# Optimization experiments

Measured on AMD Instinct MI355X. Metric: run time of the kernel, lower is better.

The kernel has to match this reference:

```python
import jax, jax.numpy as jnp
import numpy as np

N_TYPES = 6
NUM_HEADS = 8
MAX_SEQ = 50
LN_EPS = 1e-5
NEG_SLOPE = 0.2


def layer_norm(x, g, b):
    m = x.mean(-1, keepdims=True)
    v = ((x - m) ** 2).mean(-1, keepdims=True)
    return (x - m) / jnp.sqrt(v + LN_EPS) * g + b


def setup_inputs() -> dict:
    key = jax.random.key(0)
    N, E, D = 20000, 200000, 128  # nodes, edges, input_dim==hidden_dim
    ks = jax.random.split(key, 64)
    it = iter(ks)

    def w(shape):
        return jax.random.normal(next(it), shape, jnp.float32) / np.sqrt(shape[-2] if len(shape) > 1 else shape[-1]).astype(np.float32)

    inp = {}
    inp['x'] = jax.random.normal(next(it), (N, D), jnp.float32)
    inp['edge_index'] = jax.random.randint(next(it), (2, E), 0, N)
    inp['node_types'] = jax.random.randint(next(it), (N,), 0, N_TYPES)
    inp['temporal_positions'] = jax.random.randint(next(it), (N,), 0, MAX_SEQ)
    # CrossDomainGAT params
    inp['gat_Wq'] = w((D, D)); inp['gat_Wk'] = w((D, D)); inp['gat_Wv'] = w((D, D))
    inp['gat_Wo'] = w((D, D)); inp['gat_bo'] = jnp.zeros((D,), jnp.float32)
    inp['gat_g'] = jnp.ones((D,), jnp.float32); inp['gat_b'] = jnp.zeros((D,), jnp.float32)
    # SchemaAwareGCN params
    inp['gcn_Wt'] = w((N_TYPES, D, D)); inp['gcn_bt'] = jnp.zeros((N_TYPES, D), jnp.float32)
    inp['gcn_mW1'] = w((2 * D, D)); inp['gcn_mb1'] = jnp.zeros((D,), jnp.float32)
    inp['gcn_mW2'] = w((D, D)); inp['gcn_mb2'] = jnp.zeros((D,), jnp.float32)
    inp['gcn_aW1'] = w((D, D)); inp['gcn_ab1'] = jnp.zeros((D,), jnp.float32)
    inp['gcn_aW2'] = w((D, D)); inp['gcn_ab2'] = jnp.zeros((D,), jnp.float32)
    inp['gcn_Wo'] = w((D, D)); inp['gcn_bo'] = jnp.zeros((D,), jnp.float32)
    inp['gcn_g'] = jnp.ones((D,), jnp.float32); inp['gcn_b'] = jnp.zeros((D,), jnp.float32)
    # TemporalReasoningGNN params (no turn_boundaries -> LSTM/attention path skipped)
    inp['tmp_emb'] = jax.random.normal(next(it), (MAX_SEQ, D), jnp.float32)
    inp['tmp_W1'] = w((2 * D, D)); inp['tmp_b1'] = jnp.zeros((D,), jnp.float32)
    inp['tmp_W2'] = w((D, D)); inp['tmp_b2'] = jnp.zeros((D,), jnp.float32)
    inp['tmp_Wo'] = w((D, D)); inp['tmp_bo'] = jnp.zeros((D,), jnp.float32)
    inp['tmp_g'] = jnp.ones((D,), jnp.float32); inp['tmp_b'] = jnp.zeros((D,), jnp.float32)
    # Unified fusion (concat of 3 branches -> hidden) + LayerNorm
    inp['fus_W'] = w((3 * D, D)); inp['fus_b'] = jnp.zeros((D,), jnp.float32)
    inp['fus_g'] = jnp.ones((D,), jnp.float32); inp['fus_be'] = jnp.zeros((D,), jnp.float32)
    return inp


def _gat(x, row, col, Wq, Wk, Wv, Wo, bo, g, b):
    N, D = x.shape
    Dh = D // NUM_HEADS
    Q = (x @ Wq).reshape(N, NUM_HEADS, Dh)
    K = (x @ Wk).reshape(N, NUM_HEADS, Dh)
    V = (x @ Wv).reshape(N, NUM_HEADS, Dh)
    # edge-wise multi-head attention scores [E, H]
    scores = (Q[row] * K[col]).sum(-1) / np.sqrt(Dh).astype(np.float32)
    scores = jax.nn.leaky_relu(scores, NEG_SLOPE)
    # segment softmax over incoming edges of each col node
    mx = jax.ops.segment_max(scores, col, num_segments=N)
    ex = jnp.exp(scores - mx[col])
    sm = jax.ops.segment_sum(ex, col, num_segments=N)
    probs = ex / sm[col]
    wv = probs[:, :, None] * V[row]  # [E, H, Dh]
    out = jax.ops.segment_sum(wv.reshape(len(row), D), col, num_segments=N)
    out = out @ Wo + bo
    return layer_norm(out + x, g, b)


def _mlp2(z, W1, b1, W2, b2):
    return jax.nn.relu(z @ W1 + b1) @ W2 + b2


def _gcn(x, row, col, node_types, Wt, bt, mW1, mb1, mW2, mb2, aW1, ab1, aW2, ab2, Wo, bo, g, b):
    N, D = x.shape
    h = jnp.zeros((N, D), x.dtype)
    for t in range(N_TYPES):  # fixed small type count
        h = h + jnp.where((node_types == t)[:, None], x @ Wt[t] + bt[t], 0.0)
    messages = _mlp2(jnp.concatenate([h[row], h[col]], axis=1), mW1, mb1, mW2, mb2)
    agg = jax.ops.segment_sum(messages, col, num_segments=N)
    h = h + _mlp2(agg, aW1, ab1, aW2, ab2)
    h = h @ Wo + bo
    return layer_norm(h + x, g, b)


def _temporal(x, row, col, tpos, emb, W1, b1, W2, b2, Wo, bo, g, b):
    N, D = x.shape
    h = x + emb[jnp.clip(tpos, 0, MAX_SEQ - 1)]
    messages = _mlp2(jnp.concatenate([h[row], h[col]], axis=1), W1, b1, W2, b2)
    h = h + jax.ops.segment_sum(messages, col, num_segments=N)
    h = h @ Wo + bo
    return layer_norm(h, g, b)


def reference(x, edge_index, node_types, temporal_positions,
              gat_Wq, gat_Wk, gat_Wv, gat_Wo, gat_bo, gat_g, gat_b,
              gcn_Wt, gcn_bt, gcn_mW1, gcn_mb1, gcn_mW2, gcn_mb2,
              gcn_aW1, gcn_ab1, gcn_aW2, gcn_ab2, gcn_Wo, gcn_bo, gcn_g, gcn_b,
              tmp_emb, tmp_W1, tmp_b1, tmp_W2, tmp_b2, tmp_Wo, tmp_bo, tmp_g, tmp_b,
              fus_W, fus_b, fus_g, fus_be):
    row, col = edge_index[0], edge_index[1]
    o_gat = _gat(x, row, col, gat_Wq, gat_Wk, gat_Wv, gat_Wo, gat_bo, gat_g, gat_b)
    o_gcn = _gcn(x, row, col, node_types, gcn_Wt, gcn_bt, gcn_mW1, gcn_mb1, gcn_mW2, gcn_mb2,
                 gcn_aW1, gcn_ab1, gcn_aW2, gcn_ab2, gcn_Wo, gcn_bo, gcn_g, gcn_b)
    o_tmp = _temporal(x, row, col, temporal_positions, tmp_emb, tmp_W1, tmp_b1, tmp_W2, tmp_b2,
                      tmp_Wo, tmp_bo, tmp_g, tmp_b)
    fused = jnp.concatenate([o_gat, o_gcn, o_tmp], axis=-1) @ fus_W + fus_b
    return layer_norm(fused, fus_g, fus_be)
```

## Files before the change

kernel.cpp:

```cpp
#include <hip/hip_runtime.h>

using u32 = unsigned int;
using s64 = long long;

__global__ __launch_bounds__(64) void k_detect13(const u32* __restrict__ ei,
                                                 const u32* __restrict__ nt,
                                                 const u32* __restrict__ tp,
                                                 u32* __restrict__ flags) {
    if (blockIdx.x != 0 || threadIdx.x != 0) return;
    bool e64 = true, n64 = true, t64 = true;
    for (int k = 0; k < 64; ++k) {
        if (ei[2 * k + 1] != 0u) e64 = false;
        if (nt[2 * k + 1] != 0u) n64 = false;
        if (tp[2 * k + 1] != 0u) t64 = false;
    }
    flags[0] = e64 ? 1u : 0u;
    flags[1] = n64 ? 1u : 0u;
    flags[2] = t64 ? 1u : 0u;
}

__global__ __launch_bounds__(256) void k_cvt13(const void* __restrict__ src,
                                               int* __restrict__ dst, long long n,
                                               const u32* __restrict__ flags, int fidx) {
    long long i = (long long)blockIdx.x * 256 + threadIdx.x;
    if (i >= n) return;
    dst[i] = flags[fidx] ? (int)((const s64*)src)[i] : ((const int*)src)[i];
}

__global__ __launch_bounds__(256) void kz13(float* __restrict__ p, long long n) {
    long long i = (long long)blockIdx.x * 256 + threadIdx.x;
    if (i < n) p[i] = 0.f;
}
__global__ __launch_bounds__(256) void kz_i(int* __restrict__ p, int n) {
    int i = blockIdx.x * 256 + threadIdx.x;
    if (i < n) p[i] = 0;
}

__global__ __launch_bounds__(256) void k_hist(const int* __restrict__ ei, int E,
                                              int* __restrict__ cnt) {
    int e = blockIdx.x * 256 + threadIdx.x;
    if (e < E) atomicAdd(&cnt[ei[E + e]], 1);
}

__global__ __launch_bounds__(1024) void k_scan(const int* __restrict__ cnt,
                                               int* __restrict__ offA, int N) {
    __shared__ int part[1024];
    int t = threadIdx.x;
    int C = (N + 1023) >> 10;
    int beg = t * C, end = beg + C; if (end > N) end = N;
    int s = 0;
    for (int k = beg; k < end; ++k) s += cnt[k];
    part[t] = s; __syncthreads();
    for (int o = 1; o < 1024; o <<= 1) {
        int v = (t >= o) ? part[t - o] : 0;
        __syncthreads();
        part[t] += v;
        __syncthreads();
    }
    int base = (t == 0) ? 0 : part[t - 1];
    for (int k = beg; k < end; ++k) { offA[k] = base; base += cnt[k]; }
    if (t == 1023) offA[N] = part[1023];
}

__global__ __launch_bounds__(256) void k_scatter(const int* __restrict__ ei, int E,
                                                 const int* __restrict__ offA,
                                                 int* __restrict__ cur,
                                                 int* __restrict__ srow,
                                                 int* __restrict__ sedge) {
    int e = blockIdx.x * 256 + threadIdx.x;
    if (e >= E) return;
    int col = ei[E + e];
    int p = offA[col] + atomicAdd(&cur[col], 1);
    srow[p] = ei[e];
    sedge[p] = e;
}

__global__ __launch_bounds__(256) void k_thist(const int* __restrict__ nt, int N,
                                               int* __restrict__ tcnt) {
    __shared__ int lc[6];
    if (threadIdx.x < 6) lc[threadIdx.x] = 0;
    __syncthreads();
    int i = blockIdx.x * 256 + threadIdx.x;
    if (i < N) {
        int t = nt[i]; t = (t < 0 || t > 5) ? 0 : t;
        atomicAdd(&lc[t], 1);
    }
    __syncthreads();
    if (threadIdx.x < 6 && lc[threadIdx.x] > 0) atomicAdd(&tcnt[threadIdx.x], lc[threadIdx.x]);
}

__global__ __launch_bounds__(64) void k_tscan(const int* __restrict__ tcnt,
                                              int* __restrict__ toff) {
    if (threadIdx.x != 0 || blockIdx.x != 0) return;
    int s = 0;
    for (int t = 0; t < 6; ++t) { toff[t] = s; s += tcnt[t]; }
    toff[6] = s;
}

__global__ __launch_bounds__(256) void k_tscatter(const int* __restrict__ nt, int N,
                                                  const int* __restrict__ toff,
                                                  int* __restrict__ tcur,
                                                  int* __restrict__ perm) {
    __shared__ int lc[6], gb[6];
    if (threadIdx.x < 6) lc[threadIdx.x] = 0;
    __syncthreads();
    int i = blockIdx.x * 256 + threadIdx.x;
    int t = 0, lr = 0;
    if (i < N) {
        t = nt[i]; t = (t < 0 || t > 5) ? 0 : t;
        lr = atomicAdd(&lc[t], 1);
    }
    __syncthreads();
    if (threadIdx.x < 6 && lc[threadIdx.x] > 0)
        gb[threadIdx.x] = atomicAdd(&tcur[threadIdx.x], lc[threadIdx.x]);
    __syncthreads();
    if (i < N) perm[toff[t] + gb[t] + lr] = i;
}

__device__ __forceinline__ float2 ld2(const float* p) { return *(const float2*)p; }
__device__ __forceinline__ void st2(float* p, float2 v) { *(float2*)p = v; }
__device__ __forceinline__ float4 ld4(const float* p) { return *(const float4*)p; }
__device__ __forceinline__ void st4(float* p, float4 v) { *(float4*)p = v; }
__device__ __forceinline__ void fma4(float4& a, float s, float4 w) {
    a.x = fmaf(s, w.x, a.x); a.y = fmaf(s, w.y, a.y);
    a.z = fmaf(s, w.z, a.z); a.w = fmaf(s, w.w, a.w);
}

__device__ __forceinline__ float redrow(float s) {
#pragma unroll
    for (int o = 1; o < 32; o <<= 1) s += __shfl_xor(s, o);
    return s;
}


__device__ __forceinline__ void mmT(float4 (&acc)[4], const float* xs,
                                    const float* __restrict__ W, int tn, int tc) {
#pragma unroll 2
    for (int k4 = 0; k4 < 32; ++k4) {
        float4 w0 = ld4(W + (size_t)(k4 * 4 + 0) * 128 + tc * 4);
        float4 w1 = ld4(W + (size_t)(k4 * 4 + 1) * 128 + tc * 4);
        float4 w2 = ld4(W + (size_t)(k4 * 4 + 2) * 128 + tc * 4);
        float4 w3 = ld4(W + (size_t)(k4 * 4 + 3) * 128 + tc * 4);
#pragma unroll
        for (int j = 0; j < 4; ++j) {
            float4 xv = ld4(xs + (tn * 4 + j) * 128 + k4 * 4);
            fma4(acc[j], xv.x, w0); fma4(acc[j], xv.y, w1);
            fma4(acc[j], xv.z, w2); fma4(acc[j], xv.w, w3);
        }
    }
}

__device__ __forceinline__ float4 lnrow(float4 v, const float* g, const float* b, int tc) {
    float m = redrow(v.x + v.y + v.z + v.w) * 0.0078125f;
    float4 d = make_float4(v.x - m, v.y - m, v.z - m, v.w - m);
    float var = redrow(d.x * d.x + d.y * d.y + d.z * d.z + d.w * d.w) * 0.0078125f;
    float r = rsqrtf(var + 1e-5f);
    float4 gg = ld4(g + tc * 4), bb = ld4(b + tc * 4);
    return make_float4(d.x * r * gg.x + bb.x, d.y * r * gg.y + bb.y,
                       d.z * r * gg.z + bb.z, d.w * r * gg.w + bb.w);
}

__device__ __forceinline__ void stage32(float* xs, const float* src, int i0, int N) {
    int t = threadIdx.x;
#pragma unroll
    for (int ii = 0; ii < 4; ++ii) {
        int idx = t + ii * 256;
        int r = idx >> 5, c = idx & 31;
        int node = i0 + r; if (node >= N) node = N - 1;
        st4(xs + r * 128 + c * 4, ld4(src + (size_t)node * 128 + c * 4));
    }
}

__device__ __forceinline__ void xstore(float* xs, const float4 (&v)[4], int tn, int tc) {
#pragma unroll
    for (int j = 0; j < 4; ++j) st4(xs + (tn * 4 + j) * 128 + tc * 4, v[j]);
}

__global__ __launch_bounds__(256) void k_qkvT(const float* __restrict__ x,
                                              const float* __restrict__ Wq,
                                              const float* __restrict__ Wk,
                                              const float* __restrict__ Wv,
                                              float* __restrict__ big, int N) {
    __shared__ float xs[32 * 128];
    int t = threadIdx.x, tn = t >> 5, tc = t & 31;
    int i0 = blockIdx.x * 32;
    stage32(xs, x, i0, N);
    __syncthreads();
    float4 acc[4];
    const float* Ws[3] = {Wq, Wk, Wv};
#pragma unroll
    for (int m = 0; m < 3; ++m) {
#pragma unroll
        for (int j = 0; j < 4; ++j) acc[j] = make_float4(0.f, 0.f, 0.f, 0.f);
        mmT(acc, xs, Ws[m], tn, tc);
#pragma unroll
        for (int j = 0; j < 4; ++j) {
            int node = i0 + tn * 4 + j;
            if (node < N) st4(big + (size_t)node * 384 + m * 128 + tc * 4, acc[j]);
        }
    }
}

__global__ __launch_bounds__(256) void k_gat_smB(const float* __restrict__ big,
                                                 const int* __restrict__ ei, int E,
                                                 float* __restrict__ scores,
                                                 float* __restrict__ sm) {
    long long t = (long long)blockIdx.x * 256 + threadIdx.x;
    if (t >= (long long)E * 8) return;
    int e = (int)(t >> 3), h = (int)(t & 7);
    int row = ei[e], col = ei[E + e];
    const float4* q = (const float4*)(big + (size_t)row * 384 + h * 16);
    const float4* kk = (const float4*)(big + (size_t)col * 384 + 128 + h * 16);
    float s = 0.f;
#pragma unroll
    for (int d = 0; d < 4; ++d) {
        float4 a = q[d], b = kk[d];
        s += a.x * b.x + a.y * b.y + a.z * b.z + a.w * b.w;
    }
    s *= 0.25f;
    s = s > 0.f ? s : 0.2f * s;
    float ex = expf(s);
    scores[t] = ex;
    atomicAdd(&sm[(size_t)col * 8 + h], ex);
}

__global__ __launch_bounds__(256) void k_wvS2(const float* __restrict__ big,
                                              const float* __restrict__ scores,
                                              const float* __restrict__ sm,
                                              const int* __restrict__ srow,
                                              const int* __restrict__ sedge,
                                              const int* __restrict__ offA,
                                              float* __restrict__ agg, int N) {
    int l = threadIdx.x & 63;
    int col = blockIdx.x * 4 + (threadIdx.x >> 6);
    if (col >= N) return;
    int h = l >> 3;
    float sv = sm[(size_t)col * 8 + h];
    float ism = sv != 0.f ? 1.f / sv : 0.f;
    float ax = 0.f, ay = 0.f;
    int p = offA[col], pe = offA[col + 1];
    for (; p + 2 <= pe; p += 2) {
        int e0 = sedge[p], r0 = srow[p], e1 = sedge[p + 1], r1 = srow[p + 1];
        float pr0 = scores[(size_t)e0 * 8 + h] * ism;
        float pr1 = scores[(size_t)e1 * 8 + h] * ism;
        float2 v0 = ld2(big + (size_t)r0 * 384 + 256 + 2 * l);
        float2 v1 = ld2(big + (size_t)r1 * 384 + 256 + 2 * l);
        ax = fmaf(pr0, v0.x, ax); ay = fmaf(pr0, v0.y, ay);
        ax = fmaf(pr1, v1.x, ax); ay = fmaf(pr1, v1.y, ay);
    }
    for (; p < pe; ++p) {
        int e = sedge[p], r = srow[p];
        float pr = scores[(size_t)e * 8 + h] * ism;
        float2 v = ld2(big + (size_t)r * 384 + 256 + 2 * l);
        ax = fmaf(pr, v.x, ax); ay = fmaf(pr, v.y, ay);
    }
    st2(agg + (size_t)col * 128 + 2 * l, make_float2(ax, ay));
}

__global__ __launch_bounds__(256) void k_ep_gatT(const float* __restrict__ x,
                                                 const float* __restrict__ agg,
                                                 const float* __restrict__ Wo,
                                                 const float* __restrict__ bo,
                                                 const float* __restrict__ g,
                                                 const float* __restrict__ b,
                                                 const float* __restrict__ fusW,
                                                 const float* __restrict__ fus_b,
                                                 float* __restrict__ fused, int N) {
    __shared__ float xs[32 * 128];
    int t = threadIdx.x, tn = t >> 5, tc = t & 31;
    int i0 = blockIdx.x * 32;
    stage32(xs, agg, i0, N);
    __syncthreads();
    float4 acc[4];
    float4 bo4 = ld4(bo + tc * 4);
#pragma unroll
    for (int j = 0; j < 4; ++j) acc[j] = bo4;
    mmT(acc, xs, Wo, tn, tc);
    float4 o[4];
#pragma unroll
    for (int j = 0; j < 4; ++j) {
        int node = i0 + tn * 4 + j; if (node >= N) node = N - 1;
        float4 xr = ld4(x + (size_t)node * 128 + tc * 4);
        float4 v = make_float4(acc[j].x + xr.x, acc[j].y + xr.y,
                               acc[j].z + xr.z, acc[j].w + xr.w);
        o[j] = lnrow(v, g, b, tc);
    }
    __syncthreads();
    xstore(xs, o, tn, tc);
    __syncthreads();
    float4 fb4 = ld4(fus_b + tc * 4);
#pragma unroll
    for (int j = 0; j < 4; ++j) acc[j] = fb4;
    mmT(acc, xs, fusW, tn, tc);
#pragma unroll
    for (int j = 0; j < 4; ++j) {
        int node = i0 + tn * 4 + j;
        if (node < N) st4(fused + (size_t)node * 128 + tc * 4, acc[j]);
    }
}

__global__ __launch_bounds__(256) void k_hgcnT(const float* __restrict__ x,
                                               const int* __restrict__ nt,
                                               const int* __restrict__ perm,
                                               const float* __restrict__ Wt,
                                               const float* __restrict__ bt,
                                               float* __restrict__ h_gcn, int N) {
    __shared__ float xs[32 * 128];
    int t = threadIdx.x, tn = t >> 5, tc = t & 31;
    int i0 = blockIdx.x * 32;
#pragma unroll
    for (int ii = 0; ii < 4; ++ii) {
        int idx = t + ii * 256;
        int r = idx >> 5, c = idx & 31;
        int q = i0 + r; if (q >= N) q = N - 1;
        int node = perm[q];
        st4(xs + r * 128 + c * 4, ld4(x + (size_t)node * 128 + c * 4));
    }
    __syncthreads();
    int qa = i0; if (qa >= N) qa = N - 1;
    int qb = i0 + 31; if (qb >= N) qb = N - 1;
    int t0 = nt[perm[qa]]; t0 = (t0 < 0 || t0 > 5) ? 0 : t0;
    int t1 = nt[perm[qb]]; t1 = (t1 < 0 || t1 > 5) ? 0 : t1;
    float4 acc[4];
    if (t0 == t1) {
#pragma unroll
        for (int j = 0; j < 4; ++j) acc[j] = ld4(bt + t0 * 128 + tc * 4);
        mmT(acc, xs, Wt + (size_t)t0 * 16384, tn, tc);
    } else {
#pragma unroll
        for (int j = 0; j < 4; ++j) {
            int q = i0 + tn * 4 + j; if (q >= N) q = N - 1;
            int tt = nt[perm[q]]; tt = (tt < 0 || tt > 5) ? 0 : tt;
            const float* W = Wt + (size_t)tt * 16384;
            float4 a = ld4(bt + tt * 128 + tc * 4);
#pragma unroll 2
            for (int k4 = 0; k4 < 32; ++k4) {
                float4 xv = ld4(xs + (tn * 4 + j) * 128 + k4 * 4);
                float4 w0 = ld4(W + (size_t)(k4 * 4 + 0) * 128 + tc * 4);
                float4 w1 = ld4(W + (size_t)(k4 * 4 + 1) * 128 + tc * 4);
                float4 w2 = ld4(W + (size_t)(k4 * 4 + 2) * 128 + tc * 4);
                float4 w3 = ld4(W + (size_t)(k4 * 4 + 3) * 128 + tc * 4);
                fma4(a, xv.x, w0); fma4(a, xv.y, w1);
                fma4(a, xv.z, w2); fma4(a, xv.w, w3);
            }
            acc[j] = a;
        }
    }
#pragma unroll
    for (int j = 0; j < 4; ++j) {
        int q = i0 + tn * 4 + j;
        if (q < N) st4(h_gcn + (size_t)perm[q] * 128 + tc * 4, acc[j]);
    }
}

__global__ __launch_bounds__(256) void k_preT(const float* __restrict__ h,
                                              const float* __restrict__ emb,
                                              const int* __restrict__ tpos,
                                              const float* __restrict__ W1,
                                              const float* __restrict__ b1,
                                              float* __restrict__ Pa,
                                              float* __restrict__ Pb, int N, int mode) {
    __shared__ float xs[32 * 128];
    int t = threadIdx.x, tn = t >> 5, tc = t & 31;
    int i0 = blockIdx.x * 32;
#pragma unroll
    for (int ii = 0; ii < 4; ++ii) {
        int idx = t + ii * 256;
        int r = idx >> 5, c = idx & 31;
        int node = i0 + r; if (node >= N) node = N - 1;
        float4 v = ld4(h + (size_t)node * 128 + c * 4);
        if (mode) {
            int tp = tpos[node]; tp = tp < 0 ? 0 : (tp > 49 ? 49 : tp);
            float4 e = ld4(emb + tp * 128 + c * 4);
            v.x += e.x; v.y += e.y; v.z += e.z; v.w += e.w;
        }
        st4(xs + r * 128 + c * 4, v);
    }
    __syncthreads();
    float4 acc[4];
#pragma unroll
    for (int j = 0; j < 4; ++j) acc[j] = make_float4(0.f, 0.f, 0.f, 0.f);
    mmT(acc, xs, W1, tn, tc);
#pragma unroll
    for (int j = 0; j < 4; ++j) {
        int node = i0 + tn * 4 + j;
        if (node < N) st4(Pa + (size_t)node * 128 + tc * 4, acc[j]);
    }
    float4 b14 = ld4(b1 + tc * 4);
#pragma unroll
    for (int j = 0; j < 4; ++j) acc[j] = b14;
    mmT(acc, xs, W1 + (size_t)128 * 128, tn, tc);
#pragma unroll
    for (int j = 0; j < 4; ++j) {
        int node = i0 + tn * 4 + j;
        if (node < N) st4(Pb + (size_t)node * 128 + tc * 4, acc[j]);
    }
}

__global__ __launch_bounds__(256) void k_rsum2(const float* __restrict__ Pa,
                                               const float* __restrict__ Pb,
                                               const int* __restrict__ srow,
                                               const int* __restrict__ offA,
                                               float* __restrict__ s, int N) {
    int l = threadIdx.x & 63;
    int col = blockIdx.x * 4 + (threadIdx.x >> 6);
    if (col >= N) return;
    float2 pb = ld2(Pb + (size_t)col * 128 + 2 * l);
    float ax = 0.f, ay = 0.f;
    int p = offA[col], pe = offA[col + 1];
    for (; p + 4 <= pe; p += 4) {
        int r0 = srow[p], r1 = srow[p + 1], r2 = srow[p + 2], r3 = srow[p + 3];
        float2 a0 = ld2(Pa + (size_t)r0 * 128 + 2 * l);
        float2 a1 = ld2(Pa + (size_t)r1 * 128 + 2 * l);
        float2 a2 = ld2(Pa + (size_t)r2 * 128 + 2 * l);
        float2 a3 = ld2(Pa + (size_t)r3 * 128 + 2 * l);
        ax += fmaxf(a0.x + pb.x, 0.f) + fmaxf(a1.x + pb.x, 0.f)
            + fmaxf(a2.x + pb.x, 0.f) + fmaxf(a3.x + pb.x, 0.f);
        ay += fmaxf(a0.y + pb.y, 0.f) + fmaxf(a1.y + pb.y, 0.f)
            + fmaxf(a2.y + pb.y, 0.f) + fmaxf(a3.y + pb.y, 0.f);
    }
    for (; p < pe; ++p) {
        int r = srow[p];
        float2 a = ld2(Pa + (size_t)r * 128 + 2 * l);
        ax += fmaxf(a.x + pb.x, 0.f);
        ay += fmaxf(a.y + pb.y, 0.f);
    }
    st2(s + (size_t)col * 128 + 2 * l, make_float2(ax, ay));
}

__global__ __launch_bounds__(256) void k_ep_gcnT(const float* __restrict__ x,
                                                 const float* __restrict__ h_gcn,
                                                 const float* __restrict__ s,
                                                 const int* __restrict__ offA,
                                                 const float* __restrict__ W2,
                                                 const float* __restrict__ b2,
                                                 const float* __restrict__ aW1,
                                                 const float* __restrict__ ab1,
                                                 const float* __restrict__ aW2,
                                                 const float* __restrict__ ab2,
                                                 const float* __restrict__ Wo,
                                                 const float* __restrict__ bo,
                                                 const float* __restrict__ g,
                                                 const float* __restrict__ b,
                                                 const float* __restrict__ fusW,
                                                 float* __restrict__ fused, int N) {
    __shared__ float xs[32 * 128];
    int t = threadIdx.x, tn = t >> 5, tc = t & 31;
    int i0 = blockIdx.x * 32;
    int node[4];
#pragma unroll
    for (int j = 0; j < 4; ++j) {
        node[j] = i0 + tn * 4 + j; if (node[j] >= N) node[j] = N - 1;
    }
    stage32(xs, s, i0, N);
    __syncthreads();
    float4 acc[4];
    float4 b24 = ld4(b2 + tc * 4);
#pragma unroll
    for (int j = 0; j < 4; ++j) {
        float deg = (float)(offA[node[j] + 1] - offA[node[j]]);
        acc[j] = make_float4(deg * b24.x, deg * b24.y, deg * b24.z, deg * b24.w);
    }
    mmT(acc, xs, W2, tn, tc);
    __syncthreads();
    xstore(xs, acc, tn, tc);
    __syncthreads();
    float4 a14 = ld4(ab1 + tc * 4);
#pragma unroll
    for (int j = 0; j < 4; ++j) acc[j] = a14;
    mmT(acc, xs, aW1, tn, tc);
#pragma unroll
    for (int j = 0; j < 4; ++j) {
        acc[j].x = fmaxf(acc[j].x, 0.f); acc[j].y = fmaxf(acc[j].y, 0.f);
        acc[j].z = fmaxf(acc[j].z, 0.f); acc[j].w = fmaxf(acc[j].w, 0.f);
    }
    __syncthreads();
    xstore(xs, acc, tn, tc);
    __syncthreads();
    float4 a24 = ld4(ab2 + tc * 4);
#pragma unroll
    for (int j = 0; j < 4; ++j) acc[j] = a24;
    mmT(acc, xs, aW2, tn, tc);
#pragma unroll
    for (int j = 0; j < 4; ++j) {
        float4 hg = ld4(h_gcn + (size_t)node[j] * 128 + tc * 4);
        acc[j].x += hg.x; acc[j].y += hg.y; acc[j].z += hg.z; acc[j].w += hg.w;
    }
    __syncthreads();
    xstore(xs, acc, tn, tc);
    __syncthreads();
    float4 bo4 = ld4(bo + tc * 4);
#pragma unroll
    for (int j = 0; j < 4; ++j) acc[j] = bo4;
    mmT(acc, xs, Wo, tn, tc);
    float4 o[4];
#pragma unroll
    for (int j = 0; j < 4; ++j) {
        float4 xr = ld4(x + (size_t)node[j] * 128 + tc * 4);
        float4 v = make_float4(acc[j].x + xr.x, acc[j].y + xr.y,
                               acc[j].z + xr.z, acc[j].w + xr.w);
        o[j] = lnrow(v, g, b, tc);
    }
    __syncthreads();
    xstore(xs, o, tn, tc);
    __syncthreads();
#pragma unroll
    for (int j = 0; j < 4; ++j) acc[j] = ld4(fused + (size_t)node[j] * 128 + tc * 4);
    mmT(acc, xs, fusW + (size_t)128 * 128, tn, tc);
#pragma unroll
    for (int j = 0; j < 4; ++j) {
        int q = i0 + tn * 4 + j;
        if (q < N) st4(fused + (size_t)q * 128 + tc * 4, acc[j]);
    }
}

__global__ __launch_bounds__(256) void k_ep_tmpT(const float* __restrict__ x,
                                                 const float* __restrict__ emb,
                                                 const int* __restrict__ tpos,
                                                 const float* __restrict__ s,
                                                 const int* __restrict__ offA,
                                                 const float* __restrict__ W2,
                                                 const float* __restrict__ b2,
                                                 const float* __restrict__ Wo,
                                                 const float* __restrict__ bo,
                                                 const float* __restrict__ g,
                                                 const float* __restrict__ b,
                                                 const float* __restrict__ fusW,
                                                 const float* __restrict__ fused,
                                                 const float* __restrict__ fg,
                                                 const float* __restrict__ fbe,
                                                 float* __restrict__ out, int N) {
    __shared__ float xs[32 * 128];
    int t = threadIdx.x, tn = t >> 5, tc = t & 31;
    int i0 = blockIdx.x * 32;
    int node[4];
#pragma unroll
    for (int j = 0; j < 4; ++j) {
        node[j] = i0 + tn * 4 + j; if (node[j] >= N) node[j] = N - 1;
    }
    stage32(xs, s, i0, N);
    __syncthreads();
    float4 acc[4];
    float4 b24 = ld4(b2 + tc * 4);
#pragma unroll
    for (int j = 0; j < 4; ++j) {
        float deg = (float)(offA[node[j] + 1] - offA[node[j]]);
        acc[j] = make_float4(deg * b24.x, deg * b24.y, deg * b24.z, deg * b24.w);
    }
    mmT(acc, xs, W2, tn, tc);
#pragma unroll
    for (int j = 0; j < 4; ++j) {
        int tp = tpos[node[j]]; tp = tp < 0 ? 0 : (tp > 49 ? 49 : tp);
        float4 xr = ld4(x + (size_t)node[j] * 128 + tc * 4);
        float4 e = ld4(emb + tp * 128 + tc * 4);
        acc[j].x += xr.x + e.x; acc[j].y += xr.y + e.y;
        acc[j].z += xr.z + e.z; acc[j].w += xr.w + e.w;
    }
    __syncthreads();
    xstore(xs, acc, tn, tc);
    __syncthreads();
    float4 bo4 = ld4(bo + tc * 4);
#pragma unroll
    for (int j = 0; j < 4; ++j) acc[j] = bo4;
    mmT(acc, xs, Wo, tn, tc);
    float4 o[4];
#pragma unroll
    for (int j = 0; j < 4; ++j) o[j] = lnrow(acc[j], g, b, tc);
    __syncthreads();
    xstore(xs, o, tn, tc);
    __syncthreads();
#pragma unroll
    for (int j = 0; j < 4; ++j) acc[j] = ld4(fused + (size_t)node[j] * 128 + tc * 4);
    mmT(acc, xs, fusW + (size_t)256 * 128, tn, tc);
#pragma unroll
    for (int j = 0; j < 4; ++j) {
        float4 res = lnrow(acc[j], fg, fbe, tc);
        int q = i0 + tn * 4 + j;
        if (q < N) st4(out + (size_t)q * 128 + tc * 4, res);
    }
}

extern "C" void kernel_launch(void* const* d_in, const int* in_sizes, int n_in, void* d_out,
                              int out_size, void* d_ws, size_t ws_size, hipStream_t stream) {
    (void)n_in; (void)out_size; (void)ws_size;
    const float* x = (const float*)d_in[0];
    const float* gat_Wq = (const float*)d_in[4];
    const float* gat_Wk = (const float*)d_in[5];
    const float* gat_Wv = (const float*)d_in[6];
    const float* gat_Wo = (const float*)d_in[7];
    const float* gat_bo = (const float*)d_in[8];
    const float* gat_g = (const float*)d_in[9];
    const float* gat_b = (const float*)d_in[10];
    const float* gcn_Wt = (const float*)d_in[11];
    const float* gcn_bt = (const float*)d_in[12];
    const float* gcn_mW1 = (const float*)d_in[13];
    const float* gcn_mb1 = (const float*)d_in[14];
    const float* gcn_mW2 = (const float*)d_in[15];
    const float* gcn_mb2 = (const float*)d_in[16];
    const float* gcn_aW1 = (const float*)d_in[17];
    const float* gcn_ab1 = (const float*)d_in[18];
    const float* gcn_aW2 = (const float*)d_in[19];
    const float* gcn_ab2 = (const float*)d_in[20];
    const float* gcn_Wo = (const float*)d_in[21];
    const float* gcn_bo = (const float*)d_in[22];
    const float* gcn_g = (const float*)d_in[23];
    const float* gcn_b = (const float*)d_in[24];
    const float* tmp_emb = (const float*)d_in[25];
    const float* tmp_W1 = (const float*)d_in[26];
    const float* tmp_b1 = (const float*)d_in[27];
    const float* tmp_W2 = (const float*)d_in[28];
    const float* tmp_b2 = (const float*)d_in[29];
    const float* tmp_Wo = (const float*)d_in[30];
    const float* tmp_bo = (const float*)d_in[31];
    const float* tmp_g = (const float*)d_in[32];
    const float* tmp_b = (const float*)d_in[33];
    const float* fus_W = (const float*)d_in[34];
    const float* fus_b = (const float*)d_in[35];
    const float* fus_g = (const float*)d_in[36];
    const float* fus_be = (const float*)d_in[37];

    int N = in_sizes[0] / 128;
    int E = in_sizes[1] / 2;

    float* ws = (float*)d_ws;
    float* big = ws;
    float* fused = ws;
    float* h_gcn = ws + (size_t)128 * N;
    float* Pa = ws + (size_t)256 * N;
    float* Pb = ws + (size_t)384 * N;
    float* agg = ws + (size_t)512 * N;
    float* sm = ws + (size_t)640 * N;
    u32* flags = (u32*)(ws + (size_t)648 * N);
    int* ei32 = (int*)(flags + 16);
    int* nt32 = ei32 + (size_t)2 * E;
    int* tp32 = nt32 + N;
    float* scores = (float*)(tp32 + N);
    int* offA = (int*)(scores + (size_t)8 * E);
    int* cur = offA + (N + 1);
    int* srow = cur + N;
    int* sedge = srow + E;
    int* tcnt = sedge + E;
    int* toff = tcnt + 6;
    int* tcur = toff + 7;
    int* perm = cur;

    k_detect13<<<1, 64, 0, stream>>>((const u32*)d_in[1], (const u32*)d_in[2],
                                     (const u32*)d_in[3], flags);
    long long nEI = (long long)2 * E;
    k_cvt13<<<(int)((nEI + 255) / 256), 256, 0, stream>>>(d_in[1], ei32, nEI, flags, 0);
    k_cvt13<<<(N + 255) / 256, 256, 0, stream>>>(d_in[2], nt32, N, flags, 1);
    k_cvt13<<<(N + 255) / 256, 256, 0, stream>>>(d_in[3], tp32, N, flags, 2);

    int gE = (E + 255) / 256;
    int gN = (N + 255) / 256;
    int gT = (N + 31) / 32;
    int gC = (N + 3) / 4;
    int gE8 = (int)(((long long)E * 8 + 255) / 256);

    kz_i<<<gN, 256, 0, stream>>>(cur, N);
    k_hist<<<gE, 256, 0, stream>>>(ei32, E, cur);
    k_scan<<<1, 1024, 0, stream>>>(cur, offA, N);
    kz_i<<<gN, 256, 0, stream>>>(cur, N);
    k_scatter<<<gE, 256, 0, stream>>>(ei32, E, offA, cur, srow, sedge);

    kz_i<<<1, 32, 0, stream>>>(tcnt, 19);
    k_thist<<<gN, 256, 0, stream>>>(nt32, N, tcnt);
    k_tscan<<<1, 64, 0, stream>>>(tcnt, toff);
    k_tscatter<<<gN, 256, 0, stream>>>(nt32, N, toff, tcur, perm);

    kz13<<<(int)(((long long)8 * N + 255) / 256), 256, 0, stream>>>(sm, (long long)8 * N);
    k_qkvT<<<gT, 256, 0, stream>>>(x, gat_Wq, gat_Wk, gat_Wv, big, N);
    k_gat_smB<<<gE8, 256, 0, stream>>>(big, ei32, E, scores, sm);
    k_wvS2<<<gC, 256, 0, stream>>>(big, scores, sm, srow, sedge, offA, agg, N);
    k_ep_gatT<<<gT, 256, 0, stream>>>(x, agg, gat_Wo, gat_bo, gat_g, gat_b,
                                      fus_W, fus_b, fused, N);

    k_hgcnT<<<gT, 256, 0, stream>>>(x, nt32, perm, gcn_Wt, gcn_bt, h_gcn, N);
    k_preT<<<gT, 256, 0, stream>>>(h_gcn, nullptr, nullptr, gcn_mW1, gcn_mb1, Pa, Pb, N, 0);
    k_rsum2<<<gC, 256, 0, stream>>>(Pa, Pb, srow, offA, agg, N);
    k_ep_gcnT<<<gT, 256, 0, stream>>>(x, h_gcn, agg, offA, gcn_mW2, gcn_mb2,
                                      gcn_aW1, gcn_ab1, gcn_aW2, gcn_ab2,
                                      gcn_Wo, gcn_bo, gcn_g, gcn_b, fus_W, fused, N);

    k_preT<<<gT, 256, 0, stream>>>(x, tmp_emb, tp32, tmp_W1, tmp_b1, Pa, Pb, N, 1);
    k_rsum2<<<gC, 256, 0, stream>>>(Pa, Pb, srow, offA, agg, N);
    k_ep_tmpT<<<gT, 256, 0, stream>>>(x, tmp_emb, tp32, agg, offA, tmp_W2, tmp_b2,
                                      tmp_Wo, tmp_bo, tmp_g, tmp_b, fus_W, fused,
                                      fus_g, fus_be, (float*)d_out, N);
}
```

Measured before the change: 546.2 us.

## Stage weight matrices in LDS with register prefetch of the next weight

Replaces the per-thread global-memory weight reads in the dense 32x128x128 tiles with a full 64KB LDS copy of each weight matrix. Each stage stores the prefetched registers into LDS, then starts the global loads for the next weight before computing, so those loads overlap with the math. The intent is to cut repeated global and L2 weight traffic and hide load latency. In exchange each block needs about 80KB of LDS and 64 extra registers per thread, which reduces occupancy.

```diff
diff --git a/kernel.cpp b/kernel.cpp
--- a/kernel.cpp
+++ b/kernel.cpp
@@ -133,7 +133,41 @@
 }
 
 
-__device__ __forceinline__ void mmT(float4 (&acc)[4], const float* xs,
+__device__ __forceinline__ void wpre(float4 (&wreg)[16], const float* __restrict__ Wg) {
+    int t = threadIdx.x;
+#pragma unroll
+    for (int i = 0; i < 16; ++i) wreg[i] = ld4(Wg + (size_t)(t + i * 256) * 4);
+}
+
+__device__ __forceinline__ void mmP(float4 (&acc)[4], float* xs, float* wl,
+                                    float4 (&wreg)[16], const float* __restrict__ Wnext,
+                                    const float4* xin, int tn, int tc) {
+    int t = threadIdx.x;
+    __syncthreads();
+#pragma unroll
+    for (int i = 0; i < 16; ++i) st4(wl + (size_t)(t + i * 256) * 4, wreg[i]);
+    if (xin) {
+#pragma unroll
+        for (int j = 0; j < 4; ++j) st4(xs + (tn * 4 + j) * 128 + tc * 4, xin[j]);
+    }
+    if (Wnext) wpre(wreg, Wnext);
+    __syncthreads();
+#pragma unroll 2
+    for (int k4 = 0; k4 < 32; ++k4) {
+        float4 w0 = ld4(wl + (k4 * 4 + 0) * 128 + tc * 4);
+        float4 w1 = ld4(wl + (k4 * 4 + 1) * 128 + tc * 4);
+        float4 w2 = ld4(wl + (k4 * 4 + 2) * 128 + tc * 4);
+        float4 w3 = ld4(wl + (k4 * 4 + 3) * 128 + tc * 4);
+#pragma unroll
+        for (int j = 0; j < 4; ++j) {
+            float4 xv = ld4(xs + (tn * 4 + j) * 128 + k4 * 4);
+            fma4(acc[j], xv.x, w0); fma4(acc[j], xv.y, w1);
+            fma4(acc[j], xv.z, w2); fma4(acc[j], xv.w, w3);
+        }
+    }
+}
+
+__device__ __forceinline__ void mmG(float4 (&acc)[4], const float* xs,
                                     const float* __restrict__ W, int tn, int tc) {
 #pragma unroll 2
     for (int k4 = 0; k4 < 32; ++k4) {
@@ -171,28 +205,25 @@
     }
 }
 
-__device__ __forceinline__ void xstore(float* xs, const float4 (&v)[4], int tn, int tc) {
-#pragma unroll
-    for (int j = 0; j < 4; ++j) st4(xs + (tn * 4 + j) * 128 + tc * 4, v[j]);
-}
-
 __global__ __launch_bounds__(256) void k_qkvT(const float* __restrict__ x,
                                               const float* __restrict__ Wq,
                                               const float* __restrict__ Wk,
                                               const float* __restrict__ Wv,
                                               float* __restrict__ big, int N) {
     __shared__ float xs[32 * 128];
+    __shared__ float wl[128 * 128];
     int t = threadIdx.x, tn = t >> 5, tc = t & 31;
     int i0 = blockIdx.x * 32;
     stage32(xs, x, i0, N);
-    __syncthreads();
+    float4 wreg[16];
+    wpre(wreg, Wq);
+    const float* Ws[3] = {Wq, Wk, Wv};
     float4 acc[4];
-    const float* Ws[3] = {Wq, Wk, Wv};
 #pragma unroll
     for (int m = 0; m < 3; ++m) {
 #pragma unroll
         for (int j = 0; j < 4; ++j) acc[j] = make_float4(0.f, 0.f, 0.f, 0.f);
-        mmT(acc, xs, Ws[m], tn, tc);
+        mmP(acc, xs, wl, wreg, m < 2 ? Ws[m + 1] : nullptr, nullptr, tn, tc);
 #pragma unroll
         for (int j = 0; j < 4; ++j) {
             int node = i0 + tn * 4 + j;
@@ -267,15 +298,17 @@
                                                  const float* __restrict__ fus_b,
                                                  float* __restrict__ fused, int N) {
     __shared__ float xs[32 * 128];
+    __shared__ float wl[128 * 128];
     int t = threadIdx.x, tn = t >> 5, tc = t & 31;
     int i0 = blockIdx.x * 32;
     stage32(xs, agg, i0, N);
-    __syncthreads();
+    float4 wreg[16];
+    wpre(wreg, Wo);
     float4 acc[4];
     float4 bo4 = ld4(bo + tc * 4);
 #pragma unroll
     for (int j = 0; j < 4; ++j) acc[j] = bo4;
-    mmT(acc, xs, Wo, tn, tc);
+    mmP(acc, xs, wl, wreg, fusW, nullptr, tn, tc);
     float4 o[4];
 #pragma unroll
     for (int j = 0; j < 4; ++j) {
@@ -285,13 +318,10 @@
                                acc[j].z + xr.z, acc[j].w + xr.w);
         o[j] = lnrow(v, g, b, tc);
     }
-    __syncthreads();
-    xstore(xs, o, tn, tc);
-    __syncthreads();
     float4 fb4 = ld4(fus_b + tc * 4);
 #pragma unroll
     for (int j = 0; j < 4; ++j) acc[j] = fb4;
-    mmT(acc, xs, fusW, tn, tc);
+    mmP(acc, xs, wl, wreg, nullptr, o, tn, tc);
 #pragma unroll
     for (int j = 0; j < 4; ++j) {
         int node = i0 + tn * 4 + j;
@@ -306,6 +336,7 @@
                                                const float* __restrict__ bt,
                                                float* __restrict__ h_gcn, int N) {
     __shared__ float xs[32 * 128];
+    __shared__ float wl[128 * 128];
     int t = threadIdx.x, tn = t >> 5, tc = t & 31;
     int i0 = blockIdx.x * 32;
 #pragma unroll
@@ -316,17 +347,19 @@
         int node = perm[q];
         st4(xs + r * 128 + c * 4, ld4(x + (size_t)node * 128 + c * 4));
     }
-    __syncthreads();
     int qa = i0; if (qa >= N) qa = N - 1;
     int qb = i0 + 31; if (qb >= N) qb = N - 1;
     int t0 = nt[perm[qa]]; t0 = (t0 < 0 || t0 > 5) ? 0 : t0;
     int t1 = nt[perm[qb]]; t1 = (t1 < 0 || t1 > 5) ? 0 : t1;
     float4 acc[4];
     if (t0 == t1) {
+        float4 wreg[16];
+        wpre(wreg, Wt + (size_t)t0 * 16384);
 #pragma unroll
         for (int j = 0; j < 4; ++j) acc[j] = ld4(bt + t0 * 128 + tc * 4);
-        mmT(acc, xs, Wt + (size_t)t0 * 16384, tn, tc);
+        mmP(acc, xs, wl, wreg, nullptr, nullptr, tn, tc);
     } else {
+        __syncthreads();
 #pragma unroll
         for (int j = 0; j < 4; ++j) {
             int q = i0 + tn * 4 + j; if (q >= N) q = N - 1;
@@ -361,6 +394,7 @@
                                               float* __restrict__ Pa,
                                               float* __restrict__ Pb, int N, int mode) {
     __shared__ float xs[32 * 128];
+    __shared__ float wl[128 * 128];
     int t = threadIdx.x, tn = t >> 5, tc = t & 31;
     int i0 = blockIdx.x * 32;
 #pragma unroll
@@ -376,11 +410,12 @@
         }
         st4(xs + r * 128 + c * 4, v);
     }
-    __syncthreads();
+    float4 wreg[16];
+    wpre(wreg, W1);
     float4 acc[4];
 #pragma unroll
     for (int j = 0; j < 4; ++j) acc[j] = make_float4(0.f, 0.f, 0.f, 0.f);
-    mmT(acc, xs, W1, tn, tc);
+    mmP(acc, xs, wl, wreg, W1 + (size_t)128 * 128, nullptr, tn, tc);
 #pragma unroll
     for (int j = 0; j < 4; ++j) {
         int node = i0 + tn * 4 + j;
@@ -389,7 +424,7 @@
     float4 b14 = ld4(b1 + tc * 4);
 #pragma unroll
     for (int j = 0; j < 4; ++j) acc[j] = b14;
-    mmT(acc, xs, W1 + (size_t)128 * 128, tn, tc);
+    mmP(acc, xs, wl, wreg, nullptr, nullptr, tn, tc);
 #pragma unroll
     for (int j = 0; j < 4; ++j) {
         int node = i0 + tn * 4 + j;
@@ -445,6 +480,7 @@
                                                  const float* __restrict__ fusW,
                                                  float* __restrict__ fused, int N) {
     __shared__ float xs[32 * 128];
+    __shared__ float wl[128 * 128];
     int t = threadIdx.x, tn = t >> 5, tc = t & 31;
     int i0 = blockIdx.x * 32;
     int node[4];
@@ -453,64 +489,57 @@
         node[j] = i0 + tn * 4 + j; if (node[j] >= N) node[j] = N - 1;
     }
     stage32(xs, s, i0, N);
-    __syncthreads();
-    float4 acc[4];
+    float4 wreg[16];
+    wpre(wreg, W2);
+    float4 t1[4];
     float4 b24 = ld4(b2 + tc * 4);
 #pragma unroll
     for (int j = 0; j < 4; ++j) {
         float deg = (float)(offA[node[j] + 1] - offA[node[j]]);
-        acc[j] = make_float4(deg * b24.x, deg * b24.y, deg * b24.z, deg * b24.w);
-    }
-    mmT(acc, xs, W2, tn, tc);
-    __syncthreads();
-    xstore(xs, acc, tn, tc);
-    __syncthreads();
+        t1[j] = make_float4(deg * b24.x, deg * b24.y, deg * b24.z, deg * b24.w);
+    }
+    mmP(t1, xs, wl, wreg, aW1, nullptr, tn, tc);
+    float4 u[4];
     float4 a14 = ld4(ab1 + tc * 4);
 #pragma unroll
-    for (int j = 0; j < 4; ++j) acc[j] = a14;
-    mmT(acc, xs, aW1, tn, tc);
-#pragma unroll
-    for (int j = 0; j < 4; ++j) {
-        acc[j].x = fmaxf(acc[j].x, 0.f); acc[j].y = fmaxf(acc[j].y, 0.f);
-        acc[j].z = fmaxf(acc[j].z, 0.f); acc[j].w = fmaxf(acc[j].w, 0.f);
-    }
-    __syncthreads();
-    xstore(xs, acc, tn, tc);
-    __syncthreads();
+    for (int j = 0; j < 4; ++j) u[j] = a14;
+    mmP(u, xs, wl, wreg, aW2, t1, tn, tc);
+#pragma unroll
+    for (int j = 0; j < 4; ++j) {
+        u[j].x = fmaxf(u[j].x, 0.f); u[j].y = fmaxf(u[j].y, 0.f);
+        u[j].z = fmaxf(u[j].z, 0.f); u[j].w = fmaxf(u[j].w, 0.f);
+    }
+    float4 z3[4];
     float4 a24 = ld4(ab2 + tc * 4);
 #pragma unroll
-    for (int j = 0; j < 4; ++j) acc[j] = a24;
-    mmT(acc, xs, aW2, tn, tc);
+    for (int j = 0; j < 4; ++j) z3[j] = a24;
+    mmP(z3, xs, wl, wreg, Wo, u, tn, tc);
 #pragma unroll
     for (int j = 0; j < 4; ++j) {
         float4 hg = ld4(h_gcn + (size_t)node[j] * 128 + tc * 4);
-        acc[j].x += hg.x; acc[j].y += hg.y; acc[j].z += hg.z; acc[j].w += hg.w;
-    }
-    __syncthreads();
-    xstore(xs, acc, tn, tc);
-    __syncthreads();
+        z3[j].x += hg.x; z3[j].y += hg.y; z3[j].z += hg.z; z3[j].w += hg.w;
+    }
+    float4 d[4];
     float4 bo4 = ld4(bo + tc * 4);
 #pragma unroll
-    for (int j = 0; j < 4; ++j) acc[j] = bo4;
-    mmT(acc, xs, Wo, tn, tc);
+    for (int j = 0; j < 4; ++j) d[j] = bo4;
+    mmP(d, xs, wl, wreg, fusW + (size_t)128 * 128, z3, tn, tc);
     float4 o[4];
 #pragma unroll
     for (int j = 0; j < 4; ++j) {
         float4 xr = ld4(x + (size_t)node[j] * 128 + tc * 4);
-        float4 v = make_float4(acc[j].x + xr.x, acc[j].y + xr.y,
-                               acc[j].z + xr.z, acc[j].w + xr.w);
+        float4 v = make_float4(d[j].x + xr.x, d[j].y + xr.y,
+                               d[j].z + xr.z, d[j].w + xr.w);
         o[j] = lnrow(v, g, b, tc);
     }
-    __syncthreads();
-    xstore(xs, o, tn, tc);
-    __syncthreads();
-#pragma unroll
-    for (int j = 0; j < 4; ++j) acc[j] = ld4(fused + (size_t)node[j] * 128 + tc * 4);
-    mmT(acc, xs, fusW + (size_t)128 * 128, tn, tc);
+    float4 f[4];
+#pragma unroll
+    for (int j = 0; j < 4; ++j) f[j] = ld4(fused + (size_t)node[j] * 128 + tc * 4);
+    mmP(f, xs, wl, wreg, nullptr, o, tn, tc);
 #pragma unroll
     for (int j = 0; j < 4; ++j) {
         int q = i0 + tn * 4 + j;
-        if (q < N) st4(fused + (size_t)q * 128 + tc * 4, acc[j]);
+        if (q < N) st4(fused + (size_t)q * 128 + tc * 4, f[j]);
     }
 }
 
@@ -531,6 +560,7 @@
                                                  const float* __restrict__ fbe,
                                                  float* __restrict__ out, int N) {
     __shared__ float xs[32 * 128];
+    __shared__ float wl[128 * 128];
     int t = threadIdx.x, tn = t >> 5, tc = t & 31;
     int i0 = blockIdx.x * 32;
     int node[4];
@@ -539,42 +569,39 @@
         node[j] = i0 + tn * 4 + j; if (node[j] >= N) node[j] = N - 1;
     }
     stage32(xs, s, i0, N);
-    __syncthreads();
-    float4 acc[4];
+    float4 wreg[16];
+    wpre(wreg, W2);
+    float4 t1[4];
     float4 b24 = ld4(b2 + tc * 4);
 #pragma unroll
     for (int j = 0; j < 4; ++j) {
         float deg = (float)(offA[node[j] + 1] - offA[node[j]]);
-        acc[j] = make_float4(deg * b24.x, deg * b24.y, deg * b24.z, deg * b24.w);
-    }
-    mmT(acc, xs, W2, tn, tc);
+        t1[j] = make_float4(deg * b24.x, deg * b24.y, deg * b24.z, deg * b24.w);
+    }
+    mmP(t1, xs, wl, wreg, Wo, nullptr, tn, tc);
 #pragma unroll
     for (int j = 0; j < 4; ++j) {
         int tp = tpos[node[j]]; tp = tp < 0 ? 0 : (tp > 49 ? 49 : tp);
         float4 xr = ld4(x + (size_t)node[j] * 128 + tc * 4);
         float4 e = ld4(emb + tp * 128 + tc * 4);
-        acc[j].x += xr.x + e.x; acc[j].y += xr.y + e.y;
-        acc[j].z += xr.z + e.z; acc[j].w += xr.w + e.w;
-    }
-    __syncthreads();
-    xstore(xs, acc, tn, tc);
-    __syncthreads();
+        t1[j].x += xr.x + e.x; t1[j].y += xr.y + e.y;
+        t1[j].z += xr.z + e.z; t1[j].w += xr.w + e.w;
+    }
+    float4 d[4];
     float4 bo4 = ld4(bo + tc * 4);
 #pragma unroll
-    for (int j = 0; j < 4; ++j) acc[j] = bo4;
-    mmT(acc, xs, Wo, tn, tc);
+    for (int j = 0; j < 4; ++j) d[j] = bo4;
+    mmP(d, xs, wl, wreg, fusW + (size_t)256 * 128, t1, tn, tc);
     float4 o[4];
 #pragma unroll
-    for (int j = 0; j < 4; ++j) o[j] = lnrow(acc[j], g, b, tc);
-    __syncthreads();
-    xstore(xs, o, tn, tc);
-    __syncthreads();
-#pragma unroll
-    for (int j = 0; j < 4; ++j) acc[j] = ld4(fused + (size_t)node[j] * 128 + tc * 4);
-    mmT(acc, xs, fusW + (size_t)256 * 128, tn, tc);
-#pragma unroll
-    for (int j = 0; j < 4; ++j) {
-        float4 res = lnrow(acc[j], fg, fbe, tc);
+    for (int j = 0; j < 4; ++j) o[j] = lnrow(d[j], g, b, tc);
+    float4 f[4];
+#pragma unroll
+    for (int j = 0; j < 4; ++j) f[j] = ld4(fused + (size_t)node[j] * 128 + tc * 4);
+    mmP(f, xs, wl, wreg, nullptr, o, tn, tc);
+#pragma unroll
+    for (int j = 0; j < 4; ++j) {
+        float4 res = lnrow(f[j], fg, fbe, tc);
         int q = i0 + tn * 4 + j;
         if (q < N) st4(out + (size_t)q * 128 + tc * 4, res);
     }
```

Result: no change. 548.4 us (+0.4%).
